# Kernel optimization log

Measured on AMD Instinct MI355X. Metric: run time of the kernel, lower is better.

Reference implementation:

```python
import jax, jax.numpy as jnp
import numpy as np

N_NODES = 100000
N_EDGES = 1600000
D = 128


def _gcn_layer(h, W, b, src, dst, src_norm, dst_norm, n_nodes, relu):
    # DGL GraphConv norm='both': weight first (in>=out path), then normalized sparse agg
    h = h @ W                                   # [N, out]
    msg = (h * src_norm[:, None])[src]          # gather pre-normalized src feats, [E, out]
    agg = jax.ops.segment_sum(msg, dst, num_segments=n_nodes)  # scatter-add to dst
    out = agg * dst_norm[:, None] + b
    return jnp.maximum(out, 0.0) if relu else out


def setup_inputs() -> dict:
    key = jax.random.key(0)
    ks = jax.random.split(key, 10)
    feats = jax.random.normal(ks[0], (N_NODES, D), dtype=jnp.float32)
    src = jax.random.randint(ks[1], (N_EDGES,), 0, N_NODES, dtype=jnp.int64)
    dst = jax.random.randint(ks[2], (N_EDGES,), 0, N_NODES, dtype=jnp.int64)
    s = 1.0 / np.sqrt(D)
    W1 = jax.random.uniform(ks[3], (D, D), jnp.float32, -s, s)
    b1 = jnp.zeros((D,), jnp.float32)
    W2 = jax.random.uniform(ks[4], (D, D), jnp.float32, -s, s)
    b2 = jnp.zeros((D,), jnp.float32)
    W3 = jax.random.uniform(ks[5], (D, D), jnp.float32, -s, s)
    b3 = jnp.zeros((D,), jnp.float32)
    return {"feats": feats, "W1": W1, "b1": b1, "W2": W2, "b2": b2,
            "W3": W3, "b3": b3, "src": src, "dst": dst}


def reference(feats, W1, b1, W2, b2, W3, b3, src, dst):
    n = feats.shape[0]
    ones = jnp.ones(src.shape[0], dtype=feats.dtype)
    out_deg = jnp.maximum(jax.ops.segment_sum(ones, src, num_segments=n), 1.0)
    in_deg = jnp.maximum(jax.ops.segment_sum(ones, dst, num_segments=n), 1.0)
    src_norm = jax.lax.rsqrt(out_deg)
    dst_norm = jax.lax.rsqrt(in_deg)
    h = _gcn_layer(feats, W1, b1, src, dst, src_norm, dst_norm, n, relu=True)
    # dropout layers are identity in eval mode
    h = _gcn_layer(h, W2, b2, src, dst, src_norm, dst_norm, n, relu=True)
    h = _gcn_layer(h, W3, b3, src, dst, src_norm, dst_norm, n, relu=False)
    return h
```

## Files before the change

### kernel.cpp

```cpp
#include <hip/hip_runtime.h>

#define FD 128
#define DMAX 48

typedef _Float16 h16;
struct alignas(16) h8 { h16 v[8]; };

template <typename OT>
__device__ __forceinline__ void gemm_from_lds(float (*As)[FD + 4],
    const float* __restrict__ W, const int* __restrict__ outd,
    OT* __restrict__ out, int n, int row0, bool scale) {
  int j = threadIdx.x & 127;
  int rg = (threadIdx.x >> 7) * 16;
  float acc[16];
  #pragma unroll
  for (int r = 0; r < 16; r++) acc[r] = 0.0f;
  for (int k = 0; k < FD; k += 4) {
    float w0 = W[(k + 0) * FD + j];
    float w1 = W[(k + 1) * FD + j];
    float w2 = W[(k + 2) * FD + j];
    float w3 = W[(k + 3) * FD + j];
    #pragma unroll
    for (int r = 0; r < 16; r++) {
      float4 a = *(const float4*)&As[rg + r][k];
      acc[r] = fmaf(a.x, w0, acc[r]);
      acc[r] = fmaf(a.y, w1, acc[r]);
      acc[r] = fmaf(a.z, w2, acc[r]);
      acc[r] = fmaf(a.w, w3, acc[r]);
    }
  }
  #pragma unroll
  for (int r = 0; r < 16; r++) {
    int gr = row0 + rg + r;
    if (gr < n) {
      float s = 1.0f;
      if (scale) {
        int od = outd[gr]; if (od < 1) od = 1;
        s = rsqrtf((float)od);
      }
      out[(size_t)gr * FD + j] = (OT)(acc[r] * s);
    }
  }
}

__global__ __launch_bounds__(256) void k_mega(const float* __restrict__ feats,
    const float* __restrict__ W1, h16* __restrict__ msg,
    const int* __restrict__ src, const int* __restrict__ dst,
    int* __restrict__ outd, int* __restrict__ cnt, int* __restrict__ ss,
    int n, int nE, int nG) {
  __shared__ float As[32][FD + 4];
  int bid = blockIdx.x;
  if (bid % 3 == 0) {
    int g = bid / 3;
    if (g >= nG) return;
    int row0 = g * 32;
    for (int t = threadIdx.x; t < 32 * (FD / 4); t += 256) {
      int r = t >> 5, c4 = t & 31;
      int gr = row0 + r;
      float4 v = (gr < n) ? ((const float4*)feats)[(size_t)gr * 32 + c4]
                          : make_float4(0.f, 0.f, 0.f, 0.f);
      *(float4*)&As[r][c4 * 4] = v;
    }
    __syncthreads();
    gemm_from_lds<h16>(As, W1, nullptr, msg, n, row0, false);
  } else {
    int f = bid - 1 - bid / 3;
    int nF = 2 * nG;
    for (int e = f * 256 + threadIdx.x; e < nE; e += nF * 256) {
      atomicAdd(&outd[src[e]], 1);
      int d = dst[e];
      int p = atomicAdd(&cnt[d], 1);
      if (p < DMAX) ss[(size_t)d * DMAX + p] = src[e];
    }
  }
}

template <bool EDGE_SCALE>
__device__ __forceinline__ void agg_node16(const h8* __restrict__ msg8,
    const int* __restrict__ ss, int tc,
    const int* __restrict__ outd, int q, float a[8]) {
  #pragma unroll
  for (int j = 0; j < 8; j++) a[j] = 0.0f;
  int len = tc < DMAX ? tc : DMAX;
  const int* base = ss;
  int k = 0;
  for (; k + 4 <= len; k += 4) {
    int4 i4 = *(const int4*)(base + k);
    h8 w0 = msg8[(size_t)i4.x * 16 + q];
    h8 w1 = msg8[(size_t)i4.y * 16 + q];
    h8 w2 = msg8[(size_t)i4.z * 16 + q];
    h8 w3 = msg8[(size_t)i4.w * 16 + q];
    float s0 = 1.f, s1 = 1.f, s2 = 1.f, s3 = 1.f;
    if (EDGE_SCALE) {
      int o0 = outd[i4.x], o1 = outd[i4.y], o2 = outd[i4.z], o3 = outd[i4.w];
      s0 = rsqrtf((float)(o0 < 1 ? 1 : o0));
      s1 = rsqrtf((float)(o1 < 1 ? 1 : o1));
      s2 = rsqrtf((float)(o2 < 1 ? 1 : o2));
      s3 = rsqrtf((float)(o3 < 1 ? 1 : o3));
    }
    #pragma unroll
    for (int j = 0; j < 8; j++) {
      a[j] = fmaf((float)w0.v[j], s0, a[j]);
      a[j] = fmaf((float)w1.v[j], s1, a[j]);
      a[j] = fmaf((float)w2.v[j], s2, a[j]);
      a[j] = fmaf((float)w3.v[j], s3, a[j]);
    }
  }
  for (; k < len; k++) {
    int si = base[k];
    h8 w = msg8[(size_t)si * 16 + q];
    float s = 1.f;
    if (EDGE_SCALE) {
      int od = outd[si];
      s = rsqrtf((float)(od < 1 ? 1 : od));
    }
    #pragma unroll
    for (int j = 0; j < 8; j++) a[j] = fmaf((float)w.v[j], s, a[j]);
  }
}

template <bool EDGE_SCALE, typename OT>
__global__ __launch_bounds__(256) void k_agg_gemm(const h16* __restrict__ msg,
    const int* __restrict__ ss, const int* __restrict__ cnt,
    const int* __restrict__ outd, const float4* __restrict__ bias,
    const float* __restrict__ W, OT* __restrict__ out_msg, int n) {
  __shared__ float As[32][FD + 4];
  int row0 = blockIdx.x * 32;
  int q = threadIdx.x & 15;
  int grp = threadIdx.x >> 4;
  const h8* msg8 = (const h8*)msg;
  #pragma unroll
  for (int rr = 0; rr < 2; rr++) {
    int r = grp * 2 + rr;
    int node = row0 + r;
    float a[8];
    int tc = 0;
    if (node < n) {
      tc = cnt[node];
      agg_node16<EDGE_SCALE>(msg8, ss + (size_t)node * DMAX, tc, outd, q, a);
    } else {
      #pragma unroll
      for (int j = 0; j < 8; j++) a[j] = 0.0f;
    }
    float dn = rsqrtf((float)(tc < 1 ? 1 : tc));
    float4 b0 = bias[q * 2], b1 = bias[q * 2 + 1];
    float4 o0, o1;
    o0.x = fmaxf(fmaf(a[0], dn, b0.x), 0.f);
    o0.y = fmaxf(fmaf(a[1], dn, b0.y), 0.f);
    o0.z = fmaxf(fmaf(a[2], dn, b0.z), 0.f);
    o0.w = fmaxf(fmaf(a[3], dn, b0.w), 0.f);
    o1.x = fmaxf(fmaf(a[4], dn, b1.x), 0.f);
    o1.y = fmaxf(fmaf(a[5], dn, b1.y), 0.f);
    o1.z = fmaxf(fmaf(a[6], dn, b1.z), 0.f);
    o1.w = fmaxf(fmaf(a[7], dn, b1.w), 0.f);
    *(float4*)&As[r][q * 8 + 0] = o0;
    *(float4*)&As[r][q * 8 + 4] = o1;
  }
  __syncthreads();
  gemm_from_lds<OT>(As, W, outd, out_msg, n, row0, true);
}

__global__ __launch_bounds__(256) void k_agg_final(const h16* __restrict__ msg,
    const int* __restrict__ ss, const int* __restrict__ cnt,
    const float4* __restrict__ bias, float4* __restrict__ out, int n) {
  int idx = blockIdx.x * 256 + threadIdx.x;
  int node = idx >> 4;
  if (node >= n) return;
  int q = idx & 15;
  int tc = cnt[node];
  float a[8];
  agg_node16<false>((const h8*)msg, ss + (size_t)node * DMAX, tc, nullptr, q, a);
  float dn = rsqrtf((float)(tc < 1 ? 1 : tc));
  float4 b0 = bias[q * 2], b1 = bias[q * 2 + 1];
  float4 o0, o1;
  o0.x = fmaf(a[0], dn, b0.x);
  o0.y = fmaf(a[1], dn, b0.y);
  o0.z = fmaf(a[2], dn, b0.z);
  o0.w = fmaf(a[3], dn, b0.w);
  o1.x = fmaf(a[4], dn, b1.x);
  o1.y = fmaf(a[5], dn, b1.y);
  o1.z = fmaf(a[6], dn, b1.z);
  o1.w = fmaf(a[7], dn, b1.w);
  out[(size_t)node * 32 + q * 2 + 0] = o0;
  out[(size_t)node * 32 + q * 2 + 1] = o1;
}

extern "C" void kernel_launch(void* const* d_in, const int* in_sizes, int n_in,
                              void* d_out, int out_size, void* d_ws, size_t ws_size,
                              hipStream_t stream) {
  const float* feats = (const float*)d_in[0];
  const float* W1 = (const float*)d_in[1];
  const float* b1 = (const float*)d_in[2];
  const float* W2 = (const float*)d_in[3];
  const float* b2 = (const float*)d_in[4];
  const float* W3 = (const float*)d_in[5];
  const float* b3 = (const float*)d_in[6];
  const int* src = (const int*)d_in[7];
  const int* dst = (const int*)d_in[8];
  int n  = in_sizes[0] / FD;
  int nE = in_sizes[7];
  float* out = (float*)d_out;

  char* ws = (char*)d_ws;
  h16*   msgH1 = (h16*)ws;   ws += (size_t)n * FD * sizeof(h16);
  h16*   msgH3 = msgH1;
  h16*   msgH2 = (h16*)d_out;
  int*   outd = (int*)ws;    ws += (size_t)n * sizeof(int);
  int*   cnt  = (int*)ws;    ws += (size_t)n * sizeof(int);
  int*   ss   = (int*)ws;

  int nG = (n + 31) / 32;
  int finalGrid = (int)(((size_t)n * 16 + 255) / 256);

  hipMemsetAsync(outd, 0, 2 * (size_t)n * sizeof(int), stream);

  k_mega<<<3 * nG, 256, 0, stream>>>(feats, W1, msgH1, src, dst, outd, cnt, ss, n, nE, nG);
  k_agg_gemm<true, h16><<<nG, 256, 0, stream>>>(msgH1, ss, cnt, outd,
                                                (const float4*)b1, W2, msgH2, n);
  k_agg_gemm<false, h16><<<nG, 256, 0, stream>>>(msgH2, ss, cnt, outd,
                                                 (const float4*)b2, W3, msgH3, n);
  k_agg_final<<<finalGrid, 256, 0, stream>>>(msgH3, ss, cnt,
                                             (const float4*)b3, (float4*)out, n);
}
```

Baseline: 565.5 us.

## Use split-fp16 MFMA for the fused dense transforms instead of scalar FMA

New measurement: 490.3 us. 13.3% less time.

```diff
diff --git a/kernel.cpp b/kernel.cpp
--- a/kernel.cpp
+++ b/kernel.cpp
@@ -2,53 +2,112 @@
 
 #define FD 128
 #define DMAX 48
+#define LDA 136
 
 typedef _Float16 h16;
+typedef _Float16 v8h __attribute__((ext_vector_type(8)));
+typedef _Float16 v4h __attribute__((ext_vector_type(4)));
+typedef float    v4f __attribute__((ext_vector_type(4)));
 struct alignas(16) h8 { h16 v[8]; };
 
-template <typename OT>
-__device__ __forceinline__ void gemm_from_lds(float (*As)[FD + 4],
-    const float* __restrict__ W, const int* __restrict__ outd,
-    OT* __restrict__ out, int n, int row0, bool scale) {
-  int j = threadIdx.x & 127;
-  int rg = (threadIdx.x >> 7) * 16;
-  float acc[16];
-  #pragma unroll
-  for (int r = 0; r < 16; r++) acc[r] = 0.0f;
-  for (int k = 0; k < FD; k += 4) {
-    float w0 = W[(k + 0) * FD + j];
-    float w1 = W[(k + 1) * FD + j];
-    float w2 = W[(k + 2) * FD + j];
-    float w3 = W[(k + 3) * FD + j];
-    #pragma unroll
-    for (int r = 0; r < 16; r++) {
-      float4 a = *(const float4*)&As[rg + r][k];
-      acc[r] = fmaf(a.x, w0, acc[r]);
-      acc[r] = fmaf(a.y, w1, acc[r]);
-      acc[r] = fmaf(a.z, w2, acc[r]);
-      acc[r] = fmaf(a.w, w3, acc[r]);
-    }
-  }
-  #pragma unroll
-  for (int r = 0; r < 16; r++) {
-    int gr = row0 + rg + r;
-    if (gr < n) {
-      float s = 1.0f;
-      if (scale) {
-        int od = outd[gr]; if (od < 1) od = 1;
-        s = rsqrtf((float)od);
+__global__ __launch_bounds__(256) void k_prep(const float* __restrict__ W1,
+    const float* __restrict__ W2, const float* __restrict__ W3, h16* __restrict__ wt) {
+  int idx = blockIdx.x * 256 + threadIdx.x;
+  if (idx >= 3 * FD * FD) return;
+  int l = idx / (FD * FD);
+  int r = idx - l * FD * FD;
+  int c = r >> 7, k = r & 127;
+  const float* W = (l == 0) ? W1 : (l == 1) ? W2 : W3;
+  float v = W[k * FD + c];
+  h16 hi = (h16)v;
+  h16 lo = (h16)(v - (float)hi);
+  h16* base = wt + (size_t)l * 2 * FD * FD;
+  base[c * FD + k] = hi;
+  base[FD * FD + c * FD + k] = lo;
+}
+
+__device__ __forceinline__ void gemm_mfma(const h16 (*AsHi)[LDA], const h16 (*AsLo)[LDA],
+    const h16* __restrict__ wt, const int* __restrict__ outd,
+    h16* __restrict__ out, int n, int row0, bool scale) {
+  const int lane = threadIdx.x & 63;
+  const int wv = threadIdx.x >> 6;
+  const int lr = lane & 15;
+  const int lq = lane >> 4;
+  const int colb = wv * 32;
+  v4f acc[2][2];
+  #pragma unroll
+  for (int mi = 0; mi < 2; mi++)
+    #pragma unroll
+    for (int ni = 0; ni < 2; ni++)
+      acc[mi][ni] = (v4f){0.f, 0.f, 0.f, 0.f};
+
+  {
+    v8h a[2][4];
+    #pragma unroll
+    for (int mi = 0; mi < 2; mi++)
+      #pragma unroll
+      for (int kk = 0; kk < 4; kk++)
+        a[mi][kk] = *(const v8h*)&AsHi[mi * 16 + lr][kk * 32 + lq * 8];
+    #pragma unroll
+    for (int ni = 0; ni < 2; ni++) {
+      const h16* wc = wt + (size_t)(colb + ni * 16 + lr) * FD;
+      #pragma unroll
+      for (int kk = 0; kk < 4; kk++) {
+        v8h bh = *(const v8h*)&wc[kk * 32 + lq * 8];
+        v8h bl = *(const v8h*)&wc[FD * FD + kk * 32 + lq * 8];
+        #pragma unroll
+        for (int mi = 0; mi < 2; mi++) {
+          acc[mi][ni] = __builtin_amdgcn_mfma_f32_16x16x32_f16(a[mi][kk], bh, acc[mi][ni], 0, 0, 0);
+          acc[mi][ni] = __builtin_amdgcn_mfma_f32_16x16x32_f16(a[mi][kk], bl, acc[mi][ni], 0, 0, 0);
+        }
       }
-      out[(size_t)gr * FD + j] = (OT)(acc[r] * s);
+    }
+  }
+  {
+    v8h a[2][4];
+    #pragma unroll
+    for (int mi = 0; mi < 2; mi++)
+      #pragma unroll
+      for (int kk = 0; kk < 4; kk++)
+        a[mi][kk] = *(const v8h*)&AsLo[mi * 16 + lr][kk * 32 + lq * 8];
+    #pragma unroll
+    for (int ni = 0; ni < 2; ni++) {
+      const h16* wc = wt + (size_t)(colb + ni * 16 + lr) * FD;
+      #pragma unroll
+      for (int kk = 0; kk < 4; kk++) {
+        v8h bh = *(const v8h*)&wc[kk * 32 + lq * 8];
+        #pragma unroll
+        for (int mi = 0; mi < 2; mi++)
+          acc[mi][ni] = __builtin_amdgcn_mfma_f32_16x16x32_f16(a[mi][kk], bh, acc[mi][ni], 0, 0, 0);
+      }
+    }
+  }
+  #pragma unroll
+  for (int mi = 0; mi < 2; mi++) {
+    #pragma unroll
+    for (int i = 0; i < 4; i++) {
+      int grow = row0 + mi * 16 + lq * 4 + i;
+      if (grow < n) {
+        float s = 1.0f;
+        if (scale) {
+          int od = outd[grow]; if (od < 1) od = 1;
+          s = rsqrtf((float)od);
+        }
+        #pragma unroll
+        for (int ni = 0; ni < 2; ni++)
+          out[(size_t)grow * FD + colb + ni * 16 + lr] = (h16)(acc[mi][ni][i] * s);
+      }
     }
   }
 }
 
 __global__ __launch_bounds__(256) void k_mega(const float* __restrict__ feats,
-    const float* __restrict__ W1, h16* __restrict__ msg,
+    const h16* __restrict__ wt1, h16* __restrict__ msg,
     const int* __restrict__ src, const int* __restrict__ dst,
     int* __restrict__ outd, int* __restrict__ cnt, int* __restrict__ ss,
     int n, int nE, int nG) {
-  __shared__ float As[32][FD + 4];
+  __shared__ __align__(16) h16 AsHi[32][LDA];
+  __shared__ __align__(16) h16 AsLo[32][LDA];
   int bid = blockIdx.x;
   if (bid % 3 == 0) {
     int g = bid / 3;
@@ -59,10 +118,14 @@
       int gr = row0 + r;
       float4 v = (gr < n) ? ((const float4*)feats)[(size_t)gr * 32 + c4]
                           : make_float4(0.f, 0.f, 0.f, 0.f);
-      *(float4*)&As[r][c4 * 4] = v;
+      v4h vh = { (h16)v.x, (h16)v.y, (h16)v.z, (h16)v.w };
+      v4h vl = { (h16)(v.x - (float)vh[0]), (h16)(v.y - (float)vh[1]),
+                 (h16)(v.z - (float)vh[2]), (h16)(v.w - (float)vh[3]) };
+      *(v4h*)&AsHi[r][c4 * 4] = vh;
+      *(v4h*)&AsLo[r][c4 * 4] = vl;
     }
     __syncthreads();
-    gemm_from_lds<h16>(As, W1, nullptr, msg, n, row0, false);
+    gemm_mfma(AsHi, AsLo, wt1, nullptr, msg, n, row0, false);
   } else {
     int f = bid - 1 - bid / 3;
     int nF = 2 * nG;
@@ -119,12 +182,13 @@
   }
 }
 
-template <bool EDGE_SCALE, typename OT>
+template <bool EDGE_SCALE>
 __global__ __launch_bounds__(256) void k_agg_gemm(const h16* __restrict__ msg,
     const int* __restrict__ ss, const int* __restrict__ cnt,
     const int* __restrict__ outd, const float4* __restrict__ bias,
-    const float* __restrict__ W, OT* __restrict__ out_msg, int n) {
-  __shared__ float As[32][FD + 4];
+    const h16* __restrict__ wt, h16* __restrict__ out_msg, int n) {
+  __shared__ __align__(16) h16 AsHi[32][LDA];
+  __shared__ __align__(16) h16 AsLo[32][LDA];
   int row0 = blockIdx.x * 32;
   int q = threadIdx.x & 15;
   int grp = threadIdx.x >> 4;
@@ -144,20 +208,27 @@
     }
     float dn = rsqrtf((float)(tc < 1 ? 1 : tc));
     float4 b0 = bias[q * 2], b1 = bias[q * 2 + 1];
-    float4 o0, o1;
-    o0.x = fmaxf(fmaf(a[0], dn, b0.x), 0.f);
-    o0.y = fmaxf(fmaf(a[1], dn, b0.y), 0.f);
-    o0.z = fmaxf(fmaf(a[2], dn, b0.z), 0.f);
-    o0.w = fmaxf(fmaf(a[3], dn, b0.w), 0.f);
-    o1.x = fmaxf(fmaf(a[4], dn, b1.x), 0.f);
-    o1.y = fmaxf(fmaf(a[5], dn, b1.y), 0.f);
-    o1.z = fmaxf(fmaf(a[6], dn, b1.z), 0.f);
-    o1.w = fmaxf(fmaf(a[7], dn, b1.w), 0.f);
-    *(float4*)&As[r][q * 8 + 0] = o0;
-    *(float4*)&As[r][q * 8 + 4] = o1;
+    float o[8];
+    o[0] = fmaxf(fmaf(a[0], dn, b0.x), 0.f);
+    o[1] = fmaxf(fmaf(a[1], dn, b0.y), 0.f);
+    o[2] = fmaxf(fmaf(a[2], dn, b0.z), 0.f);
+    o[3] = fmaxf(fmaf(a[3], dn, b0.w), 0.f);
+    o[4] = fmaxf(fmaf(a[4], dn, b1.x), 0.f);
+    o[5] = fmaxf(fmaf(a[5], dn, b1.y), 0.f);
+    o[6] = fmaxf(fmaf(a[6], dn, b1.z), 0.f);
+    o[7] = fmaxf(fmaf(a[7], dn, b1.w), 0.f);
+    v8h hh, hl;
+    #pragma unroll
+    for (int j = 0; j < 8; j++) {
+      h16 hi = (h16)o[j];
+      hh[j] = hi;
+      hl[j] = (h16)(o[j] - (float)hi);
+    }
+    *(v8h*)&AsHi[r][q * 8] = hh;
+    *(v8h*)&AsLo[r][q * 8] = hl;
   }
   __syncthreads();
-  gemm_from_lds<OT>(As, W, outd, out_msg, n, row0, true);
+  gemm_mfma(AsHi, AsLo, wt, outd, out_msg, n, row0, true);
 }
 
 __global__ __launch_bounds__(256) void k_agg_final(const h16* __restrict__ msg,
@@ -208,17 +279,19 @@
   int*   outd = (int*)ws;    ws += (size_t)n * sizeof(int);
   int*   cnt  = (int*)ws;    ws += (size_t)n * sizeof(int);
   int*   ss   = (int*)ws;
+  h16*   wt   = (h16*)((char*)d_out + (size_t)n * FD * sizeof(h16));
 
   int nG = (n + 31) / 32;
   int finalGrid = (int)(((size_t)n * 16 + 255) / 256);
 
   hipMemsetAsync(outd, 0, 2 * (size_t)n * sizeof(int), stream);
 
-  k_mega<<<3 * nG, 256, 0, stream>>>(feats, W1, msgH1, src, dst, outd, cnt, ss, n, nE, nG);
-  k_agg_gemm<true, h16><<<nG, 256, 0, stream>>>(msgH1, ss, cnt, outd,
-                                                (const float4*)b1, W2, msgH2, n);
-  k_agg_gemm<false, h16><<<nG, 256, 0, stream>>>(msgH2, ss, cnt, outd,
-                                                 (const float4*)b2, W3, msgH3, n);
+  k_prep<<<(3 * FD * FD + 255) / 256, 256, 0, stream>>>(W1, W2, W3, wt);
+  k_mega<<<3 * nG, 256, 0, stream>>>(feats, wt, msgH1, src, dst, outd, cnt, ss, n, nE, nG);
+  k_agg_gemm<true><<<nG, 256, 0, stream>>>(msgH1, ss, cnt, outd,
+                                           (const float4*)b1, wt + 2 * FD * FD, msgH2, n);
+  k_agg_gemm<false><<<nG, 256, 0, stream>>>(msgH2, ss, cnt, outd,
+                                            (const float4*)b2, wt + 4 * FD * FD, msgH3, n);
   k_agg_final<<<finalGrid, 256, 0, stream>>>(msgH3, ss, cnt,
                                              (const float4*)b3, (float4*)out, n);
 }
```
